# Performance work log

Measured on AMD Instinct MI355X. Metric: run time of the kernel, lower is better.

The kernel has to match this reference:

```python
import jax, jax.numpy as jnp
import numpy as np

IN_CAPS, IN_DIM, NUM_CAPS, DIM_CAPS = 512, 768, 16, 64
NUM_ROUTING = 3
BETA = 1.0  # config['Model']['temperature']
B = 128


def _pearson(x, y):
    # correlation along last dim (dim_caps); returns [..., ] (keepdim then squeeze(-1))
    xm = x - x.mean(axis=-1, keepdims=True)
    ym = y - y.mean(axis=-1, keepdims=True)
    num = (xm * ym).sum(axis=-1)
    den = jnp.sqrt((xm * xm).sum(axis=-1)) * jnp.sqrt((ym * ym).sum(axis=-1))
    return num / den


def _squash(s, eps=1e-8):
    sq = (s * s).sum(axis=-1, keepdims=True)
    return (sq / (1.0 + sq)) * s / jnp.sqrt(sq + eps)


def setup_inputs() -> dict:
    key = jax.random.key(0)
    k1, k2, k3 = jax.random.split(key, 3)
    m = jax.random.normal(k1, (IN_CAPS, IN_DIM), dtype=jnp.float32)
    q = jax.random.normal(k2, (B, IN_DIM), dtype=jnp.float32)
    W_w = jax.random.normal(k3, (NUM_CAPS * DIM_CAPS, IN_DIM), dtype=jnp.float32) * 0.02
    W_b = jnp.zeros((NUM_CAPS * DIM_CAPS,), dtype=jnp.float32)
    return {"m": m, "q": q, "W_w": W_w, "W_b": W_b}


def reference(m, q, W_w, W_b):
    sg = jax.lax.stop_gradient
    bq = q.shape[0]
    hat_m = (m @ W_w.T + W_b).reshape(IN_CAPS, NUM_CAPS, DIM_CAPS)
    hat_q = (q @ W_w.T + W_b).reshape(bq, NUM_CAPS, DIM_CAPS)
    # detached copies (broadcast hat_m lazily instead of materializing [B,in_caps,K,D])
    tmp_m = sg(hat_m)[None]                                   # [1, in_caps, K, D]
    tmp_q = jnp.broadcast_to(sg(hat_q)[:, None], (bq, IN_CAPS, NUM_CAPS, DIM_CAPS))
    a = jnp.zeros((bq, IN_CAPS, NUM_CAPS), dtype=q.dtype)
    p_ij = jnp.tanh(_pearson(tmp_m, tmp_q))                   # [B, in_caps, K]
    for _ in range(NUM_ROUTING - 1):
        d = jax.nn.softmax(a / BETA, axis=2)
        d_sum_p = d - p_ij
        hat_v = (tmp_m * d_sum_p[..., None]).sum(axis=1)      # [B, K, D]
        v = _squash(hat_v)
        a = a + (tmp_m * v[:, None]).sum(axis=-1)             # [B, in_caps, K]
        tmp_q = (tmp_q + v[:, None]) * 0.5
        p_ij = jnp.tanh(_pearson(tmp_m, tmp_q))
    d = jax.nn.softmax(a / BETA, axis=2)
    d_sum_p = d - p_ij
    hat_v = (hat_m[None] * d_sum_p[..., None]).sum(axis=1)    # grads flow via hat_m
    q_prime = _squash(hat_v).reshape(bq, -1)
    return q_prime
```

## Files before the change

### kernel.cpp

```cpp
#include <hip/hip_runtime.h>
#include <hip/hip_bf16.h>
#include <cstdint>
#include <cstddef>

#define IC 512
#define IDM 768
#define KC 16
#define NB 128
#define NOUT 1024

typedef __attribute__((ext_vector_type(8))) short short8v;
typedef __attribute__((ext_vector_type(4))) float f32x4;

#define MFMA __builtin_amdgcn_mfma_f32_16x16x32_bf16

static __device__ __forceinline__ unsigned fbits(float x) {
  union { float f; unsigned u; } z; z.f = x; return z.u;
}
static __device__ __forceinline__ float bf_f(ushort u) {
  union { float f; unsigned u32; } z; z.u32 = ((unsigned)u) << 16; return z.f;
}
static __device__ __forceinline__ ushort bf_rne(float x) {
  __hip_bfloat16 h = __float2bfloat16(x);
  return *reinterpret_cast<ushort*>(&h);
}
static __device__ __forceinline__ void split2(float x, ushort& h, ushort& l) {
  h = (ushort)(fbits(x) >> 16);
  const float r = x - bf_f(h);
  l = (ushort)(fbits(r) >> 16);
}
static __device__ __forceinline__ void split8(const float* p, short8v& h, short8v& l) {
  const float4 x0 = *(const float4*)p;
  const float4 x1 = *(const float4*)(p + 4);
  const float xs[8] = {x0.x, x0.y, x0.z, x0.w, x1.x, x1.y, x1.z, x1.w};
  #pragma unroll
  for (int j = 0; j < 8; ++j) {
    ushort hh, ll; split2(xs[j], hh, ll);
    h[j] = (short)hh; l[j] = (short)ll;
  }
}

struct KArgs {
  const float *m, *q, *Ww, *Wb;
  ushort *Hb, *HTb;
  float *Yf[3]; ushort *Yb[3];
  float *Vf[2]; ushort *Vb[2];
  ushort *Db[3];
  float *summT, *invxT;
  float *syT[3], *invyT[3];
  float *outp;
};

__global__ __launch_bounds__(256) void k_gemm(KArgs A)
{
  __shared__ float sred[2][2][32];
  const int t = threadIdx.x;
  const int tile = blockIdx.x;
  const int w = t >> 6, L = t & 63, c = L & 15, g = L >> 4;
  const int wr = w >> 1, wc = w & 1;
  const int rt = tile >> 4, nt = tile & 15;
  const int r0 = rt * 32, n0 = nt * 64;
  const int arow = r0 + wr * 16 + c;
  const int bcol = n0 + wc * 32 + c;
  const float* asrc = (arow < IC) ? (A.m + (size_t)arow * IDM)
                                  : (A.q + (size_t)(arow - IC) * IDM);
  const float* b0src = A.Ww + (size_t)bcol * IDM;
  const float* b1src = A.Ww + (size_t)(bcol + 16) * IDM;

  f32x4 acc0 = {}, acc1 = {};
  #pragma unroll 2
  for (int kb = 0; kb < IDM; kb += 32) {
    short8v ah, al, bh0, bl0, bh1, bl1;
    split8(asrc + kb + g * 8, ah, al);
    split8(b0src + kb + g * 8, bh0, bl0);
    split8(b1src + kb + g * 8, bh1, bl1);
    acc0 = MFMA(ah, bh0, acc0, 0, 0, 0);
    acc0 = MFMA(ah, bl0, acc0, 0, 0, 0);
    acc0 = MFMA(al, bh0, acc0, 0, 0, 0);
    acc1 = MFMA(ah, bh1, acc1, 0, 0, 0);
    acc1 = MFMA(ah, bl1, acc1, 0, 0, 0);
    acc1 = MFMA(al, bh1, acc1, 0, 0, 0);
  }

  const float bias0 = A.Wb[bcol];
  const float bias1 = A.Wb[bcol + 16];
  float v0s[4], v1s[4];
  #pragma unroll
  for (int j = 0; j < 4; ++j) { v0s[j] = acc0[j] + bias0; v1s[j] = acc1[j] + bias1; }

  #pragma unroll
  for (int j = 0; j < 4; ++j) {
    float s = v0s[j] + v1s[j];
    float q2 = v0s[j] * v0s[j] + v1s[j] * v1s[j];
    #pragma unroll
    for (int off = 1; off < 16; off <<= 1) {
      s += __shfl_xor(s, off);
      q2 += __shfl_xor(q2, off);
    }
    if (c == 0) {
      sred[wc][0][wr * 16 + 4 * g + j] = s;
      sred[wc][1][wr * 16 + 4 * g + j] = q2;
    }
  }

  ushort h0[4], h1[4];
  #pragma unroll
  for (int j = 0; j < 4; ++j) { h0[j] = bf_rne(v0s[j]); h1[j] = bf_rne(v1s[j]); }

  const int rowb = r0 + wr * 16 + 4 * g;
  if (rowb < IC) {
    #pragma unroll
    for (int j = 0; j < 4; ++j) {
      const size_t r = (size_t)(rowb + j) * NOUT;
      A.Hb[r + bcol] = h0[j];
      A.Hb[r + bcol + 16] = h1[j];
    }
    *(ushort4*)&A.HTb[(size_t)bcol * 512 + rowb] = make_ushort4(h0[0], h0[1], h0[2], h0[3]);
    *(ushort4*)&A.HTb[(size_t)(bcol + 16) * 512 + rowb] = make_ushort4(h1[0], h1[1], h1[2], h1[3]);
  } else {
    #pragma unroll
    for (int j = 0; j < 4; ++j) {
      const size_t r = (size_t)(rowb + j - IC) * NOUT;
      A.Yf[0][r + bcol] = v0s[j]; A.Yf[0][r + bcol + 16] = v1s[j];
      A.Yb[0][r + bcol] = h0[j]; A.Yb[0][r + bcol + 16] = h1[j];
    }
  }
  __syncthreads();
  if (t < 32) {
    const int row = r0 + t;
    const float s = sred[0][0][t] + sred[1][0][t];
    const float q2 = sred[0][1][t] + sred[1][1][t];
    const float inv = rsqrtf(q2 - s * s * (1.0f / 64.0f));
    if (row < IC) {
      A.summT[nt * 512 + row] = s;
      A.invxT[nt * 512 + row] = inv;
    } else {
      A.syT[0][nt * 128 + (row - IC)] = s;
      A.invyT[0][nt * 128 + (row - IC)] = inv;
    }
  }
}

template <int RR>
__global__ __launch_bounds__(1024) void k_corr(KArgs A)
{
  __shared__ float p_lds[16][256];
  __shared__ float a_lds[16][256];
  const int t = threadIdx.x;
  const int bid = blockIdx.x;
  const int it = bid & 31, bt = bid >> 5;
  const int i0 = it * 16, b0 = bt * 16;
  const int k = t >> 6, L = t & 63, c = L & 15, g = L >> 4;

  const ushort* Yb = A.Yb[RR == 0 ? 0 : (RR == 1 ? 1 : 2)];
  const ushort* Vb = A.Vb[RR == 2 ? 1 : 0];
  const float* syT = A.syT[RR == 0 ? 0 : (RR == 1 ? 1 : 2)];
  const float* invyT = A.invyT[RR == 0 ? 0 : (RR == 1 ? 1 : 2)];
  ushort* Db = A.Db[RR == 0 ? 0 : (RR == 1 ? 1 : 2)];

  const size_t koff = (size_t)k * 64 + g * 8;
  const ushort* pH = A.Hb + (size_t)(i0 + c) * NOUT + koff;
  const ushort* pY = Yb + (size_t)(b0 + c) * NOUT + koff;
  const ushort* pV = Vb + (size_t)(b0 + c) * NOUT + koff;

  f32x4 P = {}, Aa = {};
  #pragma unroll
  for (int ks = 0; ks < 64; ks += 32) {
    const short8v ah = *(const short8v*)(pH + ks);
    const short8v yh = *(const short8v*)(pY + ks);
    P = MFMA(ah, yh, P, 0, 0, 0);
    if (RR) {
      const short8v vh = *(const short8v*)(pV + ks);
      Aa = MFMA(ah, vh, Aa, 0, 0, 0);
    }
  }

  const float syb = syT[k * 128 + b0 + c];
  const float iyb = invyT[k * 128 + b0 + c];
  const f32x4 sm4 = *(const f32x4*)&A.summT[k * 512 + i0 + 4 * g];
  const f32x4 ix4 = *(const f32x4*)&A.invxT[k * 512 + i0 + 4 * g];
  f32x4 pv;
  #pragma unroll
  for (int j = 0; j < 4; ++j)
    pv[j] = tanhf((P[j] - sm4[j] * syb * (1.0f / 64.0f)) * ix4[j] * iyb);
  *(f32x4*)&p_lds[k][c * 16 + 4 * g] = pv;
  if (RR) *(f32x4*)&a_lds[k][c * 16 + 4 * g] = Aa;
  __syncthreads();

  if (t < 256) {
    const int bl = t >> 4, il = t & 15;
    const size_t dbase = (size_t)(b0 + bl) * 8192 + (size_t)(i0 + il);
    if (RR == 0) {
      #pragma unroll
      for (int kk = 0; kk < 16; ++kk)
        Db[dbase + (size_t)kk * 512] = bf_rne(0.0625f - p_lds[kk][t]);
    } else {
      float av[16];
      float mx = -1e30f;
      #pragma unroll
      for (int kk = 0; kk < 16; ++kk) { av[kk] = a_lds[kk][t]; mx = fmaxf(mx, av[kk]); }
      float s = 0.f;
      #pragma unroll
      for (int kk = 0; kk < 16; ++kk) { av[kk] = __expf(av[kk] - mx); s += av[kk]; }
      const float inv = 1.0f / s;
      #pragma unroll
      for (int kk = 0; kk < 16; ++kk)
        Db[dbase + (size_t)kk * 512] = bf_rne(av[kk] * inv - p_lds[kk][t]);
    }
  }
}

template <int R>
__global__ __launch_bounds__(256) void k_hatv(KArgs A)
{
  __shared__ float red[3][4][16];
  __shared__ float sscale[16];
  const int t = threadIdx.x;
  const int bid = blockIdx.x;
  const int w = t >> 6, L = t & 63, c = L & 15, g = L >> 4;
  const int k = bid & 15;
  const int b0 = (bid >> 4) * 16;

  const ushort* Db = A.Db[R];
  const float* Yfin = (R == 2) ? nullptr : A.Yf[R];
  float* Yfout = (R == 2) ? nullptr : A.Yf[R + 1];
  ushort* Ybout = (R == 2) ? nullptr : A.Yb[R + 1];
  const float* Vfin = (R == 1) ? A.Vf[0] : nullptr;
  float* Vfout = (R == 2) ? nullptr : A.Vf[R];
  ushort* Vbout = (R == 2) ? nullptr : A.Vb[R];
  float* syout = (R == 2) ? nullptr : A.syT[R + 1];
  float* invyout = (R == 2) ? nullptr : A.invyT[R + 1];

  const ushort* pA = Db + (size_t)(b0 + c) * 8192 + (size_t)k * 512 + g * 8;
  const ushort* pB = A.HTb + (size_t)(k * 64 + w * 16 + c) * 512 + g * 8;

  f32x4 acc = {};
  #pragma unroll 8
  for (int i = 0; i < 512; i += 32) {
    const short8v ab = *(const short8v*)(pA + i);
    const short8v bb = *(const short8v*)(pB + i);
    acc = MFMA(ab, bb, acc, 0, 0, 0);
  }

  float sq[4];
  #pragma unroll
  for (int j = 0; j < 4; ++j) {
    sq[j] = acc[j] * acc[j];
    #pragma unroll
    for (int off = 1; off < 16; off <<= 1) sq[j] += __shfl_xor(sq[j], off);
  }
  if (c == 0) {
    #pragma unroll
    for (int j = 0; j < 4; ++j) red[0][w][4 * g + j] = sq[j];
  }
  __syncthreads();
  if (t < 16) {
    const float s = red[0][0][t] + red[0][1][t] + red[0][2][t] + red[0][3][t];
    sscale[t] = (s / (1.0f + s)) * rsqrtf(s + 1e-8f);
  }
  __syncthreads();

  const int d = w * 16 + c;
  float s1[4], s2[4];
  #pragma unroll
  for (int j = 0; j < 4; ++j) {
    const int bl_ = 4 * g + j;
    const int b = b0 + bl_;
    const float v = acc[j] * sscale[bl_];
    const size_t idx = (size_t)b * NOUT + (size_t)k * 64 + d;
    if (R == 2) {
      A.outp[idx] = v;
    } else {
      const float vs = (R == 0) ? v : (Vfin[idx] + v);
      Vfout[idx] = vs;
      Vbout[idx] = bf_rne(vs);
      const float yn = (Yfin[idx] + v) * 0.5f;
      Yfout[idx] = yn;
      Ybout[idx] = bf_rne(yn);
      s1[j] = yn; s2[j] = yn * yn;
    }
  }
  if (R != 2) {
    #pragma unroll
    for (int j = 0; j < 4; ++j) {
      #pragma unroll
      for (int off = 1; off < 16; off <<= 1) {
        s1[j] += __shfl_xor(s1[j], off);
        s2[j] += __shfl_xor(s2[j], off);
      }
    }
    if (c == 0) {
      #pragma unroll
      for (int j = 0; j < 4; ++j) {
        red[1][w][4 * g + j] = s1[j];
        red[2][w][4 * g + j] = s2[j];
      }
    }
    __syncthreads();
    if (t < 16) {
      const float s = red[1][0][t] + red[1][1][t] + red[1][2][t] + red[1][3][t];
      const float q2 = red[2][0][t] + red[2][1][t] + red[2][2][t] + red[2][3][t];
      syout[k * 128 + b0 + t] = s;
      invyout[k * 128 + b0 + t] = rsqrtf(q2 - s * s * (1.0f / 64.0f));
    }
  }
}

extern "C" void kernel_launch(void* const* d_in, const int* in_sizes, int n_in,
                              void* d_out, int out_size, void* d_ws, size_t ws_size,
                              hipStream_t stream) {
  char* w = (char*)d_ws;
  KArgs A;
  A.m  = (const float*)d_in[0];
  A.q  = (const float*)d_in[1];
  A.Ww = (const float*)d_in[2];
  A.Wb = (const float*)d_in[3];
  A.Hb   = (ushort*)(w + 0);
  A.HTb  = (ushort*)(w + 1048576);
  A.Yf[0] = (float*)(w + 2097152);
  A.Yf[1] = (float*)(w + 2621440);
  A.Yf[2] = (float*)(w + 3145728);
  A.Yb[0] = (ushort*)(w + 3670016);
  A.Yb[1] = (ushort*)(w + 3932160);
  A.Yb[2] = (ushort*)(w + 4194304);
  A.Vf[0] = (float*)(w + 4456448);
  A.Vf[1] = (float*)(w + 4980736);
  A.Vb[0] = (ushort*)(w + 5505024);
  A.Vb[1] = (ushort*)(w + 5767168);
  A.Db[0] = (ushort*)(w + 6029312);
  A.Db[1] = (ushort*)(w + 8126464);
  A.Db[2] = (ushort*)(w + 10223616);
  A.summT = (float*)(w + 12320768);
  A.invxT = (float*)(w + 12353536);
  A.syT[0]   = (float*)(w + 12386304);
  A.syT[1]   = (float*)(w + 12394496);
  A.syT[2]   = (float*)(w + 12402688);
  A.invyT[0] = (float*)(w + 12410880);
  A.invyT[1] = (float*)(w + 12419072);
  A.invyT[2] = (float*)(w + 12427264);
  A.outp = (float*)d_out;

  k_gemm<<<320, 256, 0, stream>>>(A);
  k_corr<0><<<256, 1024, 0, stream>>>(A);
  k_hatv<0><<<128, 256, 0, stream>>>(A);
  k_corr<1><<<256, 1024, 0, stream>>>(A);
  k_hatv<1><<<128, 256, 0, stream>>>(A);
  k_corr<2><<<256, 1024, 0, stream>>>(A);
  k_hatv<2><<<128, 256, 0, stream>>>(A);
}
```

Before: 78.51 us.

## Drop fp32 Y/V intermediates, keep bf16 only, and remap GEMM tile order

Removes the fp32 copies of the query-side tensors Y and V. The hatv kernel now reads and updates them from their bf16 copies, and the row statistics are computed from the bf16-rounded values so they stay consistent with what the correlation kernel reads. This reduces global memory traffic and workspace size. It also remaps GEMM block indices into regions to improve L2 locality, at the cost of extra rounding error in the iterative V and Y updates.

```diff
diff --git a/kernel.cpp b/kernel.cpp
--- a/kernel.cpp
+++ b/kernel.cpp
@@ -43,8 +43,8 @@
 struct KArgs {
   const float *m, *q, *Ww, *Wb;
   ushort *Hb, *HTb;
-  float *Yf[3]; ushort *Yb[3];
-  float *Vf[2]; ushort *Vb[2];
+  ushort *Yb[3];
+  ushort *Vb[2];
   ushort *Db[3];
   float *summT, *invxT;
   float *syT[3], *invyT[3];
@@ -55,10 +55,12 @@
 {
   __shared__ float sred[2][2][32];
   const int t = threadIdx.x;
-  const int tile = blockIdx.x;
+  const int bid = blockIdx.x;
+  const int region = bid & 7, idx = bid >> 3;
+  const int rt = (region & 1) * 10 + (idx % 10);
+  const int nt = (region >> 1) * 4 + (idx / 10);
   const int w = t >> 6, L = t & 63, c = L & 15, g = L >> 4;
   const int wr = w >> 1, wc = w & 1;
-  const int rt = tile >> 4, nt = tile & 15;
   const int r0 = rt * 32, n0 = nt * 64;
   const int arow = r0 + wr * 16 + c;
   const int bcol = n0 + wc * 32 + c;
@@ -84,14 +86,18 @@
 
   const float bias0 = A.Wb[bcol];
   const float bias1 = A.Wb[bcol + 16];
-  float v0s[4], v1s[4];
-  #pragma unroll
-  for (int j = 0; j < 4; ++j) { v0s[j] = acc0[j] + bias0; v1s[j] = acc1[j] + bias1; }
-
+  ushort h0[4], h1[4];
+  float r0s[4], r1s[4];
   #pragma unroll
   for (int j = 0; j < 4; ++j) {
-    float s = v0s[j] + v1s[j];
-    float q2 = v0s[j] * v0s[j] + v1s[j] * v1s[j];
+    h0[j] = bf_rne(acc0[j] + bias0); r0s[j] = bf_f(h0[j]);
+    h1[j] = bf_rne(acc1[j] + bias1); r1s[j] = bf_f(h1[j]);
+  }
+
+  #pragma unroll
+  for (int j = 0; j < 4; ++j) {
+    float s = r0s[j] + r1s[j];
+    float q2 = r0s[j] * r0s[j] + r1s[j] * r1s[j];
     #pragma unroll
     for (int off = 1; off < 16; off <<= 1) {
       s += __shfl_xor(s, off);
@@ -102,10 +108,6 @@
       sred[wc][1][wr * 16 + 4 * g + j] = q2;
     }
   }
-
-  ushort h0[4], h1[4];
-  #pragma unroll
-  for (int j = 0; j < 4; ++j) { h0[j] = bf_rne(v0s[j]); h1[j] = bf_rne(v1s[j]); }
 
   const int rowb = r0 + wr * 16 + 4 * g;
   if (rowb < IC) {
@@ -121,8 +123,8 @@
     #pragma unroll
     for (int j = 0; j < 4; ++j) {
       const size_t r = (size_t)(rowb + j - IC) * NOUT;
-      A.Yf[0][r + bcol] = v0s[j]; A.Yf[0][r + bcol + 16] = v1s[j];
-      A.Yb[0][r + bcol] = h0[j]; A.Yb[0][r + bcol + 16] = h1[j];
+      A.Yb[0][r + bcol] = h0[j];
+      A.Yb[0][r + bcol + 16] = h1[j];
     }
   }
   __syncthreads();
@@ -222,11 +224,9 @@
   const int b0 = (bid >> 4) * 16;
 
   const ushort* Db = A.Db[R];
-  const float* Yfin = (R == 2) ? nullptr : A.Yf[R];
-  float* Yfout = (R == 2) ? nullptr : A.Yf[R + 1];
+  const ushort* Ybin = (R == 2) ? nullptr : A.Yb[R];
   ushort* Ybout = (R == 2) ? nullptr : A.Yb[R + 1];
-  const float* Vfin = (R == 1) ? A.Vf[0] : nullptr;
-  float* Vfout = (R == 2) ? nullptr : A.Vf[R];
+  const ushort* Vbin = (R == 1) ? A.Vb[0] : nullptr;
   ushort* Vbout = (R == 2) ? nullptr : A.Vb[R];
   float* syout = (R == 2) ? nullptr : A.syT[R + 1];
   float* invyout = (R == 2) ? nullptr : A.invyT[R + 1];
@@ -271,13 +271,13 @@
     if (R == 2) {
       A.outp[idx] = v;
     } else {
-      const float vs = (R == 0) ? v : (Vfin[idx] + v);
-      Vfout[idx] = vs;
+      const float vs = (R == 0) ? v : (bf_f(Vbin[idx]) + v);
       Vbout[idx] = bf_rne(vs);
-      const float yn = (Yfin[idx] + v) * 0.5f;
-      Yfout[idx] = yn;
-      Ybout[idx] = bf_rne(yn);
-      s1[j] = yn; s2[j] = yn * yn;
+      const float yn = (bf_f(Ybin[idx]) + v) * 0.5f;
+      const ushort ynb = bf_rne(yn);
+      Ybout[idx] = ynb;
+      const float ynr = bf_f(ynb);
+      s1[j] = ynr; s2[j] = ynr * ynr;
     }
   }
   if (R != 2) {
@@ -317,27 +317,22 @@
   A.Wb = (const float*)d_in[3];
   A.Hb   = (ushort*)(w + 0);
   A.HTb  = (ushort*)(w + 1048576);
-  A.Yf[0] = (float*)(w + 2097152);
-  A.Yf[1] = (float*)(w + 2621440);
-  A.Yf[2] = (float*)(w + 3145728);
-  A.Yb[0] = (ushort*)(w + 3670016);
-  A.Yb[1] = (ushort*)(w + 3932160);
-  A.Yb[2] = (ushort*)(w + 4194304);
-  A.Vf[0] = (float*)(w + 4456448);
-  A.Vf[1] = (float*)(w + 4980736);
-  A.Vb[0] = (ushort*)(w + 5505024);
-  A.Vb[1] = (ushort*)(w + 5767168);
-  A.Db[0] = (ushort*)(w + 6029312);
-  A.Db[1] = (ushort*)(w + 8126464);
-  A.Db[2] = (ushort*)(w + 10223616);
-  A.summT = (float*)(w + 12320768);
-  A.invxT = (float*)(w + 12353536);
-  A.syT[0]   = (float*)(w + 12386304);
-  A.syT[1]   = (float*)(w + 12394496);
-  A.syT[2]   = (float*)(w + 12402688);
-  A.invyT[0] = (float*)(w + 12410880);
-  A.invyT[1] = (float*)(w + 12419072);
-  A.invyT[2] = (float*)(w + 12427264);
+  A.Yb[0] = (ushort*)(w + 2097152);
+  A.Yb[1] = (ushort*)(w + 2359296);
+  A.Yb[2] = (ushort*)(w + 2621440);
+  A.Vb[0] = (ushort*)(w + 2883584);
+  A.Vb[1] = (ushort*)(w + 3145728);
+  A.Db[0] = (ushort*)(w + 3407872);
+  A.Db[1] = (ushort*)(w + 5505024);
+  A.Db[2] = (ushort*)(w + 7602176);
+  A.summT = (float*)(w + 9699328);
+  A.invxT = (float*)(w + 9732096);
+  A.syT[0]   = (float*)(w + 9764864);
+  A.syT[1]   = (float*)(w + 9773056);
+  A.syT[2]   = (float*)(w + 9781248);
+  A.invyT[0] = (float*)(w + 9789440);
+  A.invyT[1] = (float*)(w + 9797632);
+  A.invyT[2] = (float*)(w + 9805824);
   A.outp = (float*)d_out;
 
   k_gemm<<<320, 256, 0, stream>>>(A);
```

Measured after the change: 78.02 us. Within noise of the previous version (-0.6%).
